# Kernel tuning notes

Measured on AMD Instinct MI355X. Metric: run time of the kernel, lower is better.

The kernel has to match this reference:

```python
import jax, jax.numpy as jnp
import numpy as np
import math

NUM_HEADS = 16
HEAD_DIM = 64  # 1024 / 16

def setup_inputs() -> dict:
    key = jax.random.key(0)
    k1, k2, k3 = jax.random.split(key, 3)
    B, S, D = 2, 2048, 1024
    scale = 1.0 / math.sqrt(D)
    return {
        "hidden_states": jax.random.normal(k1, (B, S, D), dtype=jnp.float32),
        "attention_mask": jnp.ones((B, S), dtype=jnp.int32),
        "Wq": jax.random.normal(k2, (D, D), dtype=jnp.float32) * scale,
        "bq": jnp.zeros((D,), dtype=jnp.float32),
        "Wk": jax.random.normal(k3, (D, D), dtype=jnp.float32) * scale,
        "bk": jnp.zeros((D,), dtype=jnp.float32),
    }

def _split_heads(x):
    # [B, S, D] -> [B, H, S, dh]
    B, S, D = x.shape
    return x.reshape(B, S, NUM_HEADS, HEAD_DIM).transpose(0, 2, 1, 3)

def reference(hidden_states, attention_mask, Wq, bq, Wk, bk):
    q = _split_heads(hidden_states @ Wq + bq)           # [B,H,S,dh]
    k = _split_heads(hidden_states @ Wk + bk)           # [B,H,S,dh]
    k = jax.nn.log_sigmoid(q) + q + k                   # fused logsigmoid on q
    k = jax.nn.log_sigmoid(k)                           # second logsigmoid
    # scores = q @ (-k^T) / sqrt(dh)
    scores = -jnp.einsum('bhqd,bhkd->bhqk', q, k) / math.sqrt(HEAD_DIM)
    # mask broadcast [B,1,S,1]: masks QUERY rows (faithful to original)
    mask = (attention_mask[:, None, :, None] == 0)
    scores = jnp.where(mask, -10000.0, scores)
    probs = jax.nn.softmax(scores, axis=-1)             # [B,H,S,S]
    # note: value == query_layer in this module
    ctx = jnp.einsum('bhqk,bhkd->bhqd', probs, q)       # [B,H,S,dh]
    B, H, S, dh = ctx.shape
    return ctx.transpose(0, 2, 1, 3).reshape(B, S, H * dh)
```

## Files before the change

kernel.cpp:

```cpp
#include <hip/hip_runtime.h>
#include <hip/hip_bf16.h>
#include <math.h>

#define B_  2
#define S_  2048
#define D_  1024
#define H_  16
#define DH_ 64
#define M_  (B_ * S_)

typedef __attribute__((ext_vector_type(8))) short bf16x8;
typedef __attribute__((ext_vector_type(4))) float f32x4;

__device__ __forceinline__ float fast_exp2(float x) {
  return __builtin_amdgcn_exp2f(x);
}

__device__ __forceinline__ unsigned short f2bf(float f) {
  union { float f; unsigned u; } c; c.f = f;
  unsigned u = c.u;
  return (unsigned short)((u + 0x7FFFu + ((u >> 16) & 1u)) >> 16);
}

__device__ __forceinline__ unsigned cvtpk(float lo, float hi) {
  unsigned r;
  asm("v_cvt_pk_bf16_f32 %0, %1, %2" : "=v"(r) : "v"(lo), "v"(hi));
  return r;
}

__device__ __forceinline__ float logsig(float x) {
  const float e = __expf(-fabsf(x));
  return fminf(x, 0.f) - __logf(1.f + e);
}

__global__ __launch_bounds__(256) void prep_w(
    const float* __restrict__ Wq, const float* __restrict__ Wk,
    unsigned short* __restrict__ WqT, unsigned short* __restrict__ WkT)
{
  __shared__ unsigned short T[64][72];
  const int tid = threadIdx.x;
  const int k0 = blockIdx.x * 64;
  const int n0 = blockIdx.y * 64;
  const float* W = blockIdx.z ? Wk : Wq;
  unsigned short* WT = blockIdx.z ? WkT : WqT;

  const int kr = tid >> 2, nc = (tid & 3) * 16;
  #pragma unroll
  for (int i = 0; i < 4; i++) {
    const float4 v = *(const float4*)&W[(size_t)(k0 + kr) * D_ + n0 + nc + i * 4];
    T[nc + i * 4 + 0][kr] = f2bf(v.x);
    T[nc + i * 4 + 1][kr] = f2bf(v.y);
    T[nc + i * 4 + 2][kr] = f2bf(v.z);
    T[nc + i * 4 + 3][kr] = f2bf(v.w);
  }
  __syncthreads();
  const int nr = tid >> 2, kc = (tid & 3) * 16;
  const uint4 a = *(const uint4*)&T[nr][kc];
  const uint4 b = *(const uint4*)&T[nr][kc + 8];
  *(uint4*)&WT[(size_t)(n0 + nr) * D_ + k0 + kc] = a;
  *(uint4*)&WT[(size_t)(n0 + nr) * D_ + k0 + kc + 8] = b;
}

__global__ __launch_bounds__(512, 4) void proj_kernel(
    const float* __restrict__ hs,
    const unsigned short* __restrict__ WqT, const unsigned short* __restrict__ WkT,
    const float* __restrict__ bqv, const float* __restrict__ bkv,
    unsigned short* __restrict__ K2b, unsigned short* __restrict__ QT)
{
  __shared__ unsigned short Ash[128][72];
  __shared__ unsigned short Bsh[2][64][72];

  const int tid  = threadIdx.x;
  const int w    = tid >> 6;
  const int lane = tid & 63;
  const int quad = lane >> 4;
  const int l16  = lane & 15;
  const int m0 = blockIdx.x * 128;
  const int n0 = blockIdx.y * 64;

  float bqs[4], bks[4];
  #pragma unroll
  for (int nt = 0; nt < 4; nt++) {
    bqs[nt] = bqv[n0 + nt * 16 + l16];
    bks[nt] = bkv[n0 + nt * 16 + l16];
  }

  f32x4 accQ[4], accK[4];
  #pragma unroll
  for (int nt = 0; nt < 4; nt++) {
    accQ[nt] = (f32x4){0.f, 0.f, 0.f, 0.f};
    accK[nt] = (f32x4){0.f, 0.f, 0.f, 0.f};
  }

  const int am = tid >> 2, ac = (tid & 3) * 16;
  const int bn = tid >> 3, bc = (tid & 7) * 8;

  float4 Af[4];
  uint4 Bq, Bk;
  {
    const size_t ra = (size_t)(m0 + am) * D_ + ac;
    #pragma unroll
    for (int i = 0; i < 4; i++) Af[i] = *(const float4*)&hs[ra + i * 4];
    const size_t rb = (size_t)(n0 + bn) * D_ + bc;
    Bq = *(const uint4*)&WqT[rb];
    Bk = *(const uint4*)&WkT[rb];
  }

  for (int k0 = 0; k0 < D_; k0 += 64) {
    if (k0) __syncthreads();
    {
      uint4 t0, t1;
      t0.x = cvtpk(Af[0].x, Af[0].y);  t0.y = cvtpk(Af[0].z, Af[0].w);
      t0.z = cvtpk(Af[1].x, Af[1].y);  t0.w = cvtpk(Af[1].z, Af[1].w);
      t1.x = cvtpk(Af[2].x, Af[2].y);  t1.y = cvtpk(Af[2].z, Af[2].w);
      t1.z = cvtpk(Af[3].x, Af[3].y);  t1.w = cvtpk(Af[3].z, Af[3].w);
      *(uint4*)&Ash[am][ac]     = t0;
      *(uint4*)&Ash[am][ac + 8] = t1;
    }
    *(uint4*)&Bsh[0][bn][bc] = Bq;
    *(uint4*)&Bsh[1][bn][bc] = Bk;
    __syncthreads();

    if (k0 + 64 < D_) {
      const size_t ra = (size_t)(m0 + am) * D_ + (k0 + 64) + ac;
      #pragma unroll
      for (int i = 0; i < 4; i++) Af[i] = *(const float4*)&hs[ra + i * 4];
      const size_t rb = (size_t)(n0 + bn) * D_ + (k0 + 64) + bc;
      Bq = *(const uint4*)&WqT[rb];
      Bk = *(const uint4*)&WkT[rb];
    }

    #pragma unroll
    for (int kk = 0; kk < 2; kk++) {
      const bf16x8 af = *(const bf16x8*)&Ash[w * 16 + l16][kk * 32 + quad * 8];
      #pragma unroll
      for (int nt = 0; nt < 4; nt++) {
        const bf16x8 bq = *(const bf16x8*)&Bsh[0][nt * 16 + l16][kk * 32 + quad * 8];
        const bf16x8 bk = *(const bf16x8*)&Bsh[1][nt * 16 + l16][kk * 32 + quad * 8];
        accQ[nt] = __builtin_amdgcn_mfma_f32_16x16x32_bf16(af, bq, accQ[nt], 0, 0, 0);
        accK[nt] = __builtin_amdgcn_mfma_f32_16x16x32_bf16(af, bk, accK[nt], 0, 0, 0);
      }
    }
  }
  __syncthreads();

  unsigned short* Qt = &Bsh[0][0][0];
  #pragma unroll
  for (int nt = 0; nt < 4; nt++) {
    float qv[4];
    #pragma unroll
    for (int r = 0; r < 4; r++) {
      const float q  = accQ[nt][r] + bqs[nt];
      const float kr = accK[nt][r] + bks[nt];
      const float k2 = logsig(logsig(q) + q + kr);
      const int m = m0 + w * 16 + quad * 4 + r;
      K2b[(size_t)m * D_ + n0 + nt * 16 + l16] = f2bf(k2);
      qv[r] = q;
    }
    const ushort4 qu = {f2bf(qv[0]), f2bf(qv[1]), f2bf(qv[2]), f2bf(qv[3])};
    *(ushort4*)&Qt[(nt * 16 + l16) * 136 + w * 16 + quad * 4] = qu;
  }
  __syncthreads();
  {
    const int dr = tid >> 3, mc = (tid & 7) * 16;
    #pragma unroll
    for (int i = 0; i < 2; i++) {
      const uint4 v = *(const uint4*)&Qt[dr * 136 + mc + i * 8];
      *(uint4*)&QT[(size_t)(n0 + dr) * M_ + m0 + mc + i * 8] = v;
    }
  }
}

__global__ __launch_bounds__(1024) void attn_kernel(
    const unsigned short* __restrict__ QT,
    const unsigned short* __restrict__ K2b,
    const int* __restrict__ mask,
    float* __restrict__ out)
{
  __shared__ unsigned short Qa [256][72];
  __shared__ unsigned short K2s[64][72];
  __shared__ unsigned short Vt [64][72];
  __shared__ unsigned short Psh[16][16][72];

  const int tid  = threadIdx.x;
  const int w    = tid >> 6;
  const int lane = tid & 63;
  const int quad = lane >> 4;
  const int l16  = lane & 15;

  const int qt = blockIdx.x;
  const int bh = blockIdx.y;
  const int b = bh >> 4, h = bh & 15;
  const size_t qrow0 = (size_t)b * S_ + (size_t)qt * 256;
  const size_t krow0 = (size_t)b * S_;
  const size_t trow  = (size_t)h * 64;

  const int rr = tid >> 4, cc = (tid & 15) * 4;
  uint2 kreg, vreg;
  {
    kreg = *(const uint2*)&K2b[(krow0 + rr) * D_ + trow + cc];
    vreg = *(const uint2*)&QT [(trow + rr) * M_ + krow0 + cc];
  }

  {
    const int dr = tid >> 4, qg = tid & 15;
    const int qc = qg * 16;
    const int dcol = dr ^ ((qg & 7) << 3);
    #pragma unroll
    for (int i = 0; i < 2; i++) {
      const uint4 v = *(const uint4*)&QT[(trow + dr) * M_ + qrow0 + qc + i * 8];
      const unsigned short* p = (const unsigned short*)&v;
      #pragma unroll
      for (int j = 0; j < 8; j++) Qa[qc + i * 8 + j][dcol] = p[j];
    }
  }
  __syncthreads();

  bf16x8 qfrag[2];
  #pragma unroll
  for (int kk = 0; kk < 2; kk++)
    qfrag[kk] =
        *(const bf16x8*)&Qa[w * 16 + l16][(kk * 32 + quad * 8) ^ ((w & 7) << 3)];

  const float c2 = (mask[qrow0 + w * 16 + l16] != 0) ? -0.18033688f : 0.f;
  float rl = 0.f;

  f32x4 Ot[4];
  #pragma unroll
  for (int dt = 0; dt < 4; dt++) Ot[dt] = (f32x4){0.f, 0.f, 0.f, 0.f};

  for (int kt = 0; kt < S_ / 64; kt++) {
    __syncthreads();
    *(uint2*)&K2s[rr][cc] = kreg;
    *(uint2*)&Vt [rr][cc] = vreg;
    __syncthreads();

    if (kt + 1 < S_ / 64) {
      kreg = *(const uint2*)&K2b[(krow0 + (kt + 1) * 64 + rr) * D_ + trow + cc];
      vreg = *(const uint2*)&QT [(trow + rr) * M_ + krow0 + (kt + 1) * 64 + cc];
    }

    bf16x8 k2f[4][2], vf[4][2];
    #pragma unroll
    for (int nt = 0; nt < 4; nt++)
      #pragma unroll
      for (int kk = 0; kk < 2; kk++) {
        k2f[nt][kk] = *(const bf16x8*)&K2s[nt * 16 + l16][kk * 32 + quad * 8];
        vf[nt][kk]  = *(const bf16x8*)&Vt [nt * 16 + l16][kk * 32 + quad * 8];
      }

    f32x4 sc[4];
    #pragma unroll
    for (int nt = 0; nt < 4; nt++) sc[nt] = (f32x4){0.f, 0.f, 0.f, 0.f};
    __builtin_amdgcn_s_setprio(1);
    #pragma unroll
    for (int kk = 0; kk < 2; kk++)
      #pragma unroll
      for (int nt = 0; nt < 4; nt++)
        sc[nt] = __builtin_amdgcn_mfma_f32_16x16x32_bf16(k2f[nt][kk], qfrag[kk], sc[nt], 0, 0, 0);
    __builtin_amdgcn_s_setprio(0);

    #pragma unroll
    for (int nt = 0; nt < 4; nt++) {
      float p0 = fast_exp2(fmaf(sc[nt][0], c2, -12.f));
      float p1 = fast_exp2(fmaf(sc[nt][1], c2, -12.f));
      float p2 = fast_exp2(fmaf(sc[nt][2], c2, -12.f));
      float p3 = fast_exp2(fmaf(sc[nt][3], c2, -12.f));
      rl += (p0 + p1) + (p2 + p3);
      const uint2 pk = {cvtpk(p0, p1), cvtpk(p2, p3)};
      *(uint2*)&Psh[w][l16][nt * 16 + quad * 4] = pk;
    }

    #pragma unroll
    for (int kk = 0; kk < 2; kk++) {
      const bf16x8 pf = *(const bf16x8*)&Psh[w][l16][kk * 32 + quad * 8];
      __builtin_amdgcn_s_setprio(1);
      #pragma unroll
      for (int dt = 0; dt < 4; dt++)
        Ot[dt] = __builtin_amdgcn_mfma_f32_16x16x32_bf16(vf[dt][kk], pf, Ot[dt], 0, 0, 0);
      __builtin_amdgcn_s_setprio(0);
    }
  }

  {
    float li = rl;
    li += __shfl_xor(li, 16);
    li += __shfl_xor(li, 32);
    const float inv = 1.f / fmaxf(li, 1e-35f);
    const size_t orow = (qrow0 + w * 16 + l16) * D_ + trow;
    #pragma unroll
    for (int dt = 0; dt < 4; dt++) {
      const float4 o = {Ot[dt][0] * inv, Ot[dt][1] * inv,
                        Ot[dt][2] * inv, Ot[dt][3] * inv};
      *(float4*)&out[orow + dt * 16 + quad * 4] = o;
    }
  }
}

extern "C" void kernel_launch(void* const* d_in, const int* in_sizes, int n_in,
                              void* d_out, int out_size, void* d_ws, size_t ws_size,
                              hipStream_t stream) {
  const float* hs  = (const float*)d_in[0];
  const int*   msk = (const int*)d_in[1];
  const float* Wq  = (const float*)d_in[2];
  const float* bq  = (const float*)d_in[3];
  const float* Wk  = (const float*)d_in[4];
  const float* bk  = (const float*)d_in[5];
  float* out = (float*)d_out;

  unsigned short* QT  = (unsigned short*)d_ws;
  unsigned short* K2b = QT  + (size_t)D_ * M_;
  unsigned short* WqT = K2b + (size_t)M_ * D_;
  unsigned short* WkT = WqT + (size_t)D_ * D_;

  prep_w<<<dim3(D_ / 64, D_ / 64, 2), 256, 0, stream>>>(Wq, Wk, WqT, WkT);
  proj_kernel<<<dim3(M_ / 128, D_ / 64), 512, 0, stream>>>(hs, WqT, WkT, bq, bk, K2b, QT);
  attn_kernel<<<dim3(S_ / 256, B_ * H_), 1024, 0, stream>>>(QT, K2b, msk, out);
}
```

Baseline: 168.0 us.

## Switch attention to 32x32x16 MFMA with split-K across waves and LDS reduction

The attention kernel moves from 16x16x32 MFMA tiles to 32x32x16 tiles. Each wave now owns 32 query rows and half of every 64-key block, so waves 0-7 and 8-15 split the key dimension. Their partial outputs and row sums are combined through shared memory at the end. The aim is fewer MFMA issues and fewer fragment loads per key tile, at the cost of an extra cross-wave reduction, more barriers, and a larger accumulator footprint.

```diff
diff --git a/kernel.cpp b/kernel.cpp
--- a/kernel.cpp
+++ b/kernel.cpp
@@ -11,6 +11,7 @@
 
 typedef __attribute__((ext_vector_type(8))) short bf16x8;
 typedef __attribute__((ext_vector_type(4))) float f32x4;
+typedef __attribute__((ext_vector_type(16))) float f32x16;
 
 __device__ __forceinline__ float fast_exp2(float x) {
   return __builtin_amdgcn_exp2f(x);
@@ -180,13 +181,16 @@
   __shared__ unsigned short Qa [256][72];
   __shared__ unsigned short K2s[64][72];
   __shared__ unsigned short Vt [64][72];
-  __shared__ unsigned short Psh[16][16][72];
+  __shared__ unsigned short Psh[16][32][40];
 
   const int tid  = threadIdx.x;
   const int w    = tid >> 6;
   const int lane = tid & 63;
-  const int quad = lane >> 4;
-  const int l16  = lane & 15;
+  const int r31  = lane & 31;
+  const int hi   = lane >> 5;
+  const int hi8  = hi * 8;
+  const int qsub = w & 7;
+  const int ksel = w >> 3;
 
   const int qt = blockIdx.x;
   const int bh = blockIdx.y;
@@ -197,10 +201,8 @@
 
   const int rr = tid >> 4, cc = (tid & 15) * 4;
   uint2 kreg, vreg;
-  {
-    kreg = *(const uint2*)&K2b[(krow0 + rr) * D_ + trow + cc];
-    vreg = *(const uint2*)&QT [(trow + rr) * M_ + krow0 + cc];
-  }
+  kreg = *(const uint2*)&K2b[(krow0 + rr) * D_ + trow + cc];
+  vreg = *(const uint2*)&QT [(trow + rr) * M_ + krow0 + cc];
 
   {
     const int dr = tid >> 4, qg = tid & 15;
@@ -216,83 +218,117 @@
   }
   __syncthreads();
 
-  bf16x8 qfrag[2];
-  #pragma unroll
-  for (int kk = 0; kk < 2; kk++)
-    qfrag[kk] =
-        *(const bf16x8*)&Qa[w * 16 + l16][(kk * 32 + quad * 8) ^ ((w & 7) << 3)];
-
-  const float c2 = (mask[qrow0 + w * 16 + l16] != 0) ? -0.18033688f : 0.f;
+  bf16x8 qfrag[4];
+  {
+    const int qrow = qsub * 32 + r31;
+    const int g7 = (qrow >> 4) & 7;
+    #pragma unroll
+    for (int s = 0; s < 4; s++)
+      qfrag[s] = *(const bf16x8*)&Qa[qrow][(s * 16 + hi8) ^ (g7 << 3)];
+  }
+
+  const float c2 = (mask[qrow0 + qsub * 32 + r31] != 0) ? -0.18033688f : 0.f;
   float rl = 0.f;
 
-  f32x4 Ot[4];
-  #pragma unroll
-  for (int dt = 0; dt < 4; dt++) Ot[dt] = (f32x4){0.f, 0.f, 0.f, 0.f};
-
-  for (int kt = 0; kt < S_ / 64; kt++) {
+  f32x16 Ot0, Ot1;
+  #pragma unroll
+  for (int r = 0; r < 16; r++) { Ot0[r] = 0.f; Ot1[r] = 0.f; }
+
+  const int NT = S_ / 64;
+  for (int kt = 0; kt < NT; kt++) {
     __syncthreads();
     *(uint2*)&K2s[rr][cc] = kreg;
     *(uint2*)&Vt [rr][cc] = vreg;
     __syncthreads();
 
-    if (kt + 1 < S_ / 64) {
+    if (kt + 1 < NT) {
       kreg = *(const uint2*)&K2b[(krow0 + (kt + 1) * 64 + rr) * D_ + trow + cc];
       vreg = *(const uint2*)&QT [(trow + rr) * M_ + krow0 + (kt + 1) * 64 + cc];
     }
 
-    bf16x8 k2f[4][2], vf[4][2];
-    #pragma unroll
-    for (int nt = 0; nt < 4; nt++)
-      #pragma unroll
-      for (int kk = 0; kk < 2; kk++) {
-        k2f[nt][kk] = *(const bf16x8*)&K2s[nt * 16 + l16][kk * 32 + quad * 8];
-        vf[nt][kk]  = *(const bf16x8*)&Vt [nt * 16 + l16][kk * 32 + quad * 8];
-      }
-
-    f32x4 sc[4];
-    #pragma unroll
-    for (int nt = 0; nt < 4; nt++) sc[nt] = (f32x4){0.f, 0.f, 0.f, 0.f};
+    bf16x8 kf[4];
+    #pragma unroll
+    for (int s = 0; s < 4; s++)
+      kf[s] = *(const bf16x8*)&K2s[ksel * 32 + r31][s * 16 + hi8];
+    f32x16 sc;
+    #pragma unroll
+    for (int r = 0; r < 16; r++) sc[r] = 0.f;
     __builtin_amdgcn_s_setprio(1);
     #pragma unroll
-    for (int kk = 0; kk < 2; kk++)
-      #pragma unroll
-      for (int nt = 0; nt < 4; nt++)
-        sc[nt] = __builtin_amdgcn_mfma_f32_16x16x32_bf16(k2f[nt][kk], qfrag[kk], sc[nt], 0, 0, 0);
+    for (int s = 0; s < 4; s++)
+      sc = __builtin_amdgcn_mfma_f32_32x32x16_bf16(kf[s], qfrag[s], sc, 0, 0, 0);
     __builtin_amdgcn_s_setprio(0);
 
-    #pragma unroll
-    for (int nt = 0; nt < 4; nt++) {
-      float p0 = fast_exp2(fmaf(sc[nt][0], c2, -12.f));
-      float p1 = fast_exp2(fmaf(sc[nt][1], c2, -12.f));
-      float p2 = fast_exp2(fmaf(sc[nt][2], c2, -12.f));
-      float p3 = fast_exp2(fmaf(sc[nt][3], c2, -12.f));
-      rl += (p0 + p1) + (p2 + p3);
-      const uint2 pk = {cvtpk(p0, p1), cvtpk(p2, p3)};
-      *(uint2*)&Psh[w][l16][nt * 16 + quad * 4] = pk;
-    }
-
-    #pragma unroll
-    for (int kk = 0; kk < 2; kk++) {
-      const bf16x8 pf = *(const bf16x8*)&Psh[w][l16][kk * 32 + quad * 8];
-      __builtin_amdgcn_s_setprio(1);
-      #pragma unroll
-      for (int dt = 0; dt < 4; dt++)
-        Ot[dt] = __builtin_amdgcn_mfma_f32_16x16x32_bf16(vf[dt][kk], pf, Ot[dt], 0, 0, 0);
-      __builtin_amdgcn_s_setprio(0);
-    }
-  }
-
-  {
-    float li = rl;
-    li += __shfl_xor(li, 16);
-    li += __shfl_xor(li, 32);
-    const float inv = 1.f / fmaxf(li, 1e-35f);
-    const size_t orow = (qrow0 + w * 16 + l16) * D_ + trow;
-    #pragma unroll
-    for (int dt = 0; dt < 4; dt++) {
-      const float4 o = {Ot[dt][0] * inv, Ot[dt][1] * inv,
-                        Ot[dt][2] * inv, Ot[dt][3] * inv};
-      *(float4*)&out[orow + dt * 16 + quad * 4] = o;
+    float p[16];
+    #pragma unroll
+    for (int r = 0; r < 16; r++) p[r] = fast_exp2(fmaf(sc[r], c2, -12.f));
+    #pragma unroll
+    for (int r = 0; r < 16; r += 4) rl += ((p[r] + p[r+1]) + (p[r+2] + p[r+3]));
+    {
+      unsigned short* pr = &Psh[w][r31][0];
+      const uint2 g0 = {cvtpk(p[0],  p[1]),  cvtpk(p[2],  p[3])};
+      const uint2 g1 = {cvtpk(p[4],  p[5]),  cvtpk(p[6],  p[7])};
+      const uint2 g2 = {cvtpk(p[8],  p[9]),  cvtpk(p[10], p[11])};
+      const uint2 g3 = {cvtpk(p[12], p[13]), cvtpk(p[14], p[15])};
+      *(uint2*)&pr[ 0 + 4 * hi] = g0;
+      *(uint2*)&pr[ 8 + 4 * hi] = g1;
+      *(uint2*)&pr[16 + 4 * hi] = g2;
+      *(uint2*)&pr[24 + 4 * hi] = g3;
+    }
+
+    __builtin_amdgcn_s_setprio(1);
+    #pragma unroll
+    for (int s2 = 0; s2 < 2; s2++) {
+      const bf16x8 pf  = *(const bf16x8*)&Psh[w][r31][s2 * 16 + hi8];
+      const bf16x8 vf0 = *(const bf16x8*)&Vt[r31]     [ksel * 32 + s2 * 16 + hi8];
+      const bf16x8 vf1 = *(const bf16x8*)&Vt[32 + r31][ksel * 32 + s2 * 16 + hi8];
+      Ot0 = __builtin_amdgcn_mfma_f32_32x32x16_bf16(vf0, pf, Ot0, 0, 0, 0);
+      Ot1 = __builtin_amdgcn_mfma_f32_32x32x16_bf16(vf1, pf, Ot1, 0, 0, 0);
+    }
+    __builtin_amdgcn_s_setprio(0);
+  }
+
+  rl += __shfl_xor(rl, 32);
+  __syncthreads();
+  float* redO = (float*)&Qa[0][0];
+  float* redL = (float*)&K2s[0][0];
+  if (ksel == 1) {
+    #pragma unroll
+    for (int r = 0; r < 16; r++) redO[(qsub * 16 + r) * 64 + lane] = Ot0[r];
+    redL[qsub * 64 + lane] = rl;
+  }
+  __syncthreads();
+  float inv = 0.f;
+  size_t orow = 0;
+  if (ksel == 0) {
+    const float lt = rl + redL[qsub * 64 + lane];
+    inv = 1.f / fmaxf(lt, 1e-35f);
+    orow = (qrow0 + qsub * 32 + r31) * D_ + trow;
+    #pragma unroll
+    for (int rq = 0; rq < 4; rq++) {
+      float4 o;
+      o.x = (Ot0[4*rq+0] + redO[(qsub*16 + 4*rq+0)*64 + lane]) * inv;
+      o.y = (Ot0[4*rq+1] + redO[(qsub*16 + 4*rq+1)*64 + lane]) * inv;
+      o.z = (Ot0[4*rq+2] + redO[(qsub*16 + 4*rq+2)*64 + lane]) * inv;
+      o.w = (Ot0[4*rq+3] + redO[(qsub*16 + 4*rq+3)*64 + lane]) * inv;
+      *(float4*)&out[orow + rq * 8 + 4 * hi] = o;
+    }
+  }
+  __syncthreads();
+  if (ksel == 1) {
+    #pragma unroll
+    for (int r = 0; r < 16; r++) redO[(qsub * 16 + r) * 64 + lane] = Ot1[r];
+  }
+  __syncthreads();
+  if (ksel == 0) {
+    #pragma unroll
+    for (int rq = 0; rq < 4; rq++) {
+      float4 o;
+      o.x = (Ot1[4*rq+0] + redO[(qsub*16 + 4*rq+0)*64 + lane]) * inv;
+      o.y = (Ot1[4*rq+1] + redO[(qsub*16 + 4*rq+1)*64 + lane]) * inv;
+      o.z = (Ot1[4*rq+2] + redO[(qsub*16 + 4*rq+2)*64 + lane]) * inv;
+      o.w = (Ot1[4*rq+3] + redO[(qsub*16 + 4*rq+3)*64 + lane]) * inv;
+      *(float4*)&out[orow + 32 + rq * 8 + 4 * hi] = o;
     }
   }
 }
```

Measured after the change: 155.5 us. -7.4%, faster.
